# Optimization experiments

Hardware: AMD Instinct MI355X
Metric: run time of the kernel (lower is better)

## Reference

```python
import jax, jax.numpy as jnp
import numpy as np

B, T, X_DIM, H, Y_DIM = 64, 2048, 256, 512, 1

def _lstm_dir(x, lens, w_ih, w_hh, b_ih, b_hh, reverse):
    # x: [B, T, In]; lens: [B] int; w_ih: [4H, In]; w_hh: [4H, H]
    Bb, Tt, _ = x.shape
    Hh = w_hh.shape[-1]
    t_idx = jnp.arange(Tt)
    if reverse:
        # reverse each sequence within its valid length (pack semantics)
        ridx = jnp.clip(lens[:, None] - 1 - t_idx[None, :], 0, Tt - 1)  # [B, T]
        x = jnp.take_along_axis(x, ridx[:, :, None], axis=1)
    valid = (t_idx[None, :] < lens[:, None]).T            # [T, B]
    xT = jnp.swapaxes(x, 0, 1)                            # [T, B, In]
    # hoist the input projection out of the scan (one big GEMM)
    x_proj = jnp.einsum('tbi,gi->tbg', xT, w_ih) + b_ih + b_hh  # [T, B, 4H]
    h0 = jnp.zeros((Bb, Hh), x.dtype)
    c0 = jnp.zeros((Bb, Hh), x.dtype)

    def step(carry, inp):
        h, c = carry
        xp, m = inp                                       # [B,4H], [B]
        g = xp + h @ w_hh.T
        i, f, gg, o = jnp.split(g, 4, axis=-1)            # torch gate order i,f,g,o
        i = jax.nn.sigmoid(i); f = jax.nn.sigmoid(f)
        gg = jnp.tanh(gg); o = jax.nn.sigmoid(o)
        c_new = f * c + i * gg
        h_new = o * jnp.tanh(c_new)
        m = m[:, None]
        h = jnp.where(m, h_new, h)                        # freeze state past seq end
        c = jnp.where(m, c_new, c)
        return (h, c), h

    (h_last, _), outs = jax.lax.scan(step, (h0, c0), (x_proj, valid))
    outs = jnp.swapaxes(outs, 0, 1)                       # [B, T, H]
    if reverse:
        ridx = jnp.clip(lens[:, None] - 1 - t_idx[None, :], 0, Tt - 1)
        outs = jnp.take_along_axis(outs, ridx[:, :, None], axis=1)
    return outs, h_last


def setup_inputs() -> dict:
    key = jax.random.key(0)
    ks = jax.random.split(key, 12)
    s = 1.0 / np.sqrt(H)
    u = lambda k, shp: jax.random.uniform(k, shp, jnp.float32, -s, s)
    seqs = jax.random.normal(ks[0], (B, T, X_DIM), jnp.float32)
    lens = jax.random.randint(ks[1], (B,), 1, T + 1)
    seqs_len = jnp.sort(lens)[::-1].astype(jnp.int64)     # descending, as pack_padded requires
    return {
        'seqs': seqs, 'seqs_len': seqs_len,
        'w_ih_l0': u(ks[2], (2, 4 * H, X_DIM)),   # [dir, 4H, in]
        'w_hh_l0': u(ks[3], (2, 4 * H, H)),
        'b_ih_l0': u(ks[4], (2, 4 * H)),
        'b_hh_l0': u(ks[5], (2, 4 * H)),
        'w_ih_l1': u(ks[6], (2, 4 * H, 2 * H)),
        'w_hh_l1': u(ks[7], (2, 4 * H, H)),
        'b_ih_l1': u(ks[8], (2, 4 * H)),
        'b_hh_l1': u(ks[9], (2, 4 * H)),
        'w_out': u(ks[10], (Y_DIM, 2 * H)),
        'b_out': u(ks[11], (Y_DIM,)),
    }


def reference(seqs, seqs_len, w_ih_l0, w_hh_l0, b_ih_l0, b_hh_l0,
              w_ih_l1, w_hh_l1, b_ih_l1, b_hh_l1, w_out, b_out):
    lens = seqs_len.astype(jnp.int32)
    x = seqs
    h_f = h_b = None
    for (wi, wh, bi, bh) in ((w_ih_l0, w_hh_l0, b_ih_l0, b_hh_l0),
                             (w_ih_l1, w_hh_l1, b_ih_l1, b_hh_l1)):
        out_f, h_f = _lstm_dir(x, lens, wi[0], wh[0], bi[0], bh[0], reverse=False)
        out_b, h_b = _lstm_dir(x, lens, wi[1], wh[1], bi[1], bh[1], reverse=True)
        x = jnp.concatenate([out_f, out_b], axis=-1)      # [B, T, 2H]
    out = jnp.concatenate([h_f, h_b], axis=1)             # last-layer final hidden, [B, 2H]
    out = jax.nn.sigmoid(out @ w_out.T + b_out)           # [B, y_dim]
    return out.squeeze(-1)                                # [B]
```

## Files before the change

### kernel.cpp

```cpp
#include <hip/hip_runtime.h>
#include <stdint.h>
#include <stddef.h>

#define B_  64
#define T_  2048
#define XD  256
#define H_  512
#define G4  2048
#define BT_ (B_*T_)

typedef __attribute__((ext_vector_type(8))) _Float16 f16x8;
typedef __attribute__((ext_vector_type(4))) float f32x4;
typedef __attribute__((ext_vector_type(4))) unsigned int u32x4;
typedef __attribute__((ext_vector_type(4))) unsigned short us4;
typedef __attribute__((ext_vector_type(2))) _Float16 f16x2;

__device__ __attribute__((aligned(256))) unsigned short g_xh[(size_t)BT_*XD];
__device__ __attribute__((aligned(256))) unsigned short g_w1h[(size_t)2*G4*XD];
__device__ __attribute__((aligned(256))) unsigned short g_w2h[(size_t)2*G4*1024];
__device__ __attribute__((aligned(256))) _Float16       g_xproj[(size_t)2*BT_*G4];
__device__ __attribute__((aligned(256))) unsigned short g_out1[(size_t)BT_*1024];
__device__ __attribute__((aligned(256))) unsigned short g_hbuf[2][2][2][B_*H_];
__device__ __attribute__((aligned(256))) float          g_hlast[2][B_*H_];
__device__ __attribute__((aligned(256))) unsigned int   g_flag[2][2][64][32];

__device__ inline unsigned short f2h(float f) {
  _Float16 h = (_Float16)f;
  return __builtin_bit_cast(unsigned short, h);
}
__device__ inline float sigf(float x)  { return 1.f/(1.f + __expf(-x)); }
__device__ inline float tanh_(float x) { return 1.f - 2.f/(__expf(2.f*x) + 1.f); }

__global__ void k_init() {
  unsigned int i = blockIdx.x*256u + threadIdx.x;
  unsigned int stride = gridDim.x*256u;
  unsigned int* hb = (unsigned int*)&g_hbuf[0][0][0][0];
  for (unsigned int j = i; j < sizeof(g_hbuf)/4; j += stride) hb[j] = 0u;
  unsigned int* fl = (unsigned int*)&g_flag[0][0][0][0];
  for (unsigned int j = i; j < sizeof(g_flag)/4; j += stride) fl[j] = 0u;
}

__global__ void k_cvt_x(const float* __restrict__ src) {
  const size_t n4 = (size_t)BT_*XD/4;
  for (size_t j = (size_t)blockIdx.x*blockDim.x + threadIdx.x; j < n4;
       j += (size_t)gridDim.x*blockDim.x) {
    float4 v = ((const float4*)src)[j];
    us4 o = { f2h(v.x), f2h(v.y), f2h(v.z), f2h(v.w) };
    ((us4*)g_xh)[j] = o;
  }
}
__global__ void k_cvt_w1(const float* __restrict__ src) {
  const size_t n4 = (size_t)2*G4*XD/4;
  for (size_t j = (size_t)blockIdx.x*blockDim.x + threadIdx.x; j < n4;
       j += (size_t)gridDim.x*blockDim.x) {
    float4 v = ((const float4*)src)[j];
    us4 o = { f2h(v.x), f2h(v.y), f2h(v.z), f2h(v.w) };
    ((us4*)g_w1h)[j] = o;
  }
}
__global__ void k_cvt_w2(const float* __restrict__ src) {
  const size_t n4 = (size_t)2*G4*1024/4;
  for (size_t j = (size_t)blockIdx.x*blockDim.x + threadIdx.x; j < n4;
       j += (size_t)gridDim.x*blockDim.x) {
    float4 v = ((const float4*)src)[j];
    us4 o = { f2h(v.x), f2h(v.y), f2h(v.z), f2h(v.w) };
    ((us4*)g_w2h)[j] = o;
  }
}

template<int LAYER>
__global__ __launch_bounds__(256) void k_xproj(const float* __restrict__ b_ih,
                                               const float* __restrict__ b_hh,
                                               const int* __restrict__ lens) {
  constexpr int K = (LAYER == 0) ? XD : 1024;
  const unsigned short* __restrict__ Abf = (LAYER == 0) ? g_xh : g_out1;
  const unsigned short* __restrict__ Wbf = (LAYER == 0) ? g_w1h : g_w2h;

  const int m0 = blockIdx.x*128;
  const int n0 = blockIdx.y*128;
  const int d  = blockIdx.z;
  const int bseq = m0 / T_;
  const int t0   = m0 % T_;
  if (t0 >= lens[bseq]) return;

  __shared__ unsigned short As[128*64];
  __shared__ unsigned short Bs[128*64];

  const int tid  = threadIdx.x;
  const int lane = tid & 63;
  const int wv   = tid >> 6;
  const int moff = (wv >> 1)*64;
  const int noff = (wv & 1)*64;

  f32x4 acc[4][4] = {};

  const unsigned short* Ag = Abf + (size_t)m0*K;
  const unsigned short* Wg = Wbf + ((size_t)d*G4 + n0)*K;

  for (int k0 = 0; k0 < K; k0 += 64) {
    __syncthreads();
    #pragma unroll
    for (int p = 0; p < 4; ++p) {
      int sidx = p*256 + tid;
      int row = sidx >> 3;
      int ch  = sidx & 7;
      u32x4 va = *(const u32x4*)(Ag + (size_t)row*K + k0 + ch*8);
      u32x4 vb = *(const u32x4*)(Wg + (size_t)row*K + k0 + ch*8);
      int wb = row*128 + ((ch ^ (row & 7)) << 4);
      *(u32x4*)((char*)As + wb) = va;
      *(u32x4*)((char*)Bs + wb) = vb;
    }
    __syncthreads();
    #pragma unroll
    for (int kt = 0; kt < 2; ++kt) {
      int slot = kt*4 + (lane >> 4);
      f16x8 af[4], bfv[4];
      #pragma unroll
      for (int mt = 0; mt < 4; ++mt) {
        int r = moff + mt*16 + (lane & 15);
        af[mt] = *(const f16x8*)((const char*)As + r*128 + ((slot ^ (r & 7)) << 4));
      }
      #pragma unroll
      for (int nt = 0; nt < 4; ++nt) {
        int r = noff + nt*16 + (lane & 15);
        bfv[nt] = *(const f16x8*)((const char*)Bs + r*128 + ((slot ^ (r & 7)) << 4));
      }
      #pragma unroll
      for (int mt = 0; mt < 4; ++mt)
        #pragma unroll
        for (int nt = 0; nt < 4; ++nt)
          acc[mt][nt] = __builtin_amdgcn_mfma_f32_16x16x32_f16(af[mt], bfv[nt], acc[mt][nt], 0, 0, 0);
    }
  }

  #pragma unroll
  for (int nt = 0; nt < 4; ++nt) {
    const int col = n0 + noff + nt*16 + (lane & 15);
    const float bias = b_ih[d*G4 + col] + b_hh[d*G4 + col];
    #pragma unroll
    for (int mt = 0; mt < 4; ++mt) {
      const int row = m0 + moff + mt*16 + (lane >> 4)*4;
      _Float16* op = g_xproj + ((size_t)d*BT_ + row)*G4 + col;
      #pragma unroll
      for (int j = 0; j < 4; ++j)
        op[(size_t)j*G4] = (_Float16)(acc[mt][nt][j] + bias);
    }
  }
}

template<int LAYER>
__global__ __launch_bounds__(256, 1) void k_scan(const float* __restrict__ w_hh,
                                                 const int* __restrict__ lens) {
  const int dir  = blockIdx.x & 1;
  const int wg   = blockIdx.x >> 1;
  const int tid  = threadIdx.x;
  const int lane = tid & 63;
  const int wv   = tid >> 6;

  __shared__ unsigned short Wl[32*512];
  __shared__ float gs[64*33];

  for (int i = tid; i < 32*256; i += 256) {
    int e = i*2;
    int row = e >> 9;
    int k   = e & 511;
    int gate = row >> 3, hc = row & 7;
    int grow = gate*H_ + wg*8 + hc;
    const float* wsrc = w_hh + ((size_t)dir*G4 + grow)*H_ + k;
    unsigned int pk = (unsigned int)f2h(wsrc[0]) | ((unsigned int)f2h(wsrc[1]) << 16);
    int byte = row*1024 + ((((k*2) >> 4) ^ (row & 7)) << 4) + ((k*2) & 15);
    *(unsigned int*)((char*)Wl + byte) = pk;
  }
  __syncthreads();

  f16x8 b0r[16], b1r[16];
  {
    const int r0 = lane & 15, r1 = 16 + (lane & 15);
    #pragma unroll
    for (int kt = 0; kt < 16; ++kt) {
      int slot = kt*4 + (lane >> 4);
      b0r[kt] = *(const f16x8*)((const char*)Wl + r0*1024 + ((slot ^ (r0 & 7)) << 4));
      b1r[kt] = *(const f16x8*)((const char*)Wl + r1*1024 + ((slot ^ (r1 & 7)) << 4));
    }
  }

  const int myseq = tid >> 2;
  const int hcA   = (tid & 3)*2;
  const int mylen = lens[myseq];
  const int maxlen = lens[0];
  const int col0  = wg*8;
  const int arow  = wv*16 + (lane & 15);
  float c0 = 0.f, c1 = 0.f, h0k = 0.f, h1k = 0.f;
  unsigned int hold = 0u;

  unsigned short* hbuf0 = &g_hbuf[LAYER][dir][0][0];
  unsigned short* hbuf1 = &g_hbuf[LAYER][dir][1][0];
  unsigned int*   flags = &g_flag[LAYER][dir][0][0];

  const unsigned int h_voff  = (unsigned int)(arow*1024 + ((lane >> 4)*16));
  const unsigned int st_voff = (unsigned int)((myseq*H_ + col0 + hcA)*2);
  const unsigned int fl_voff = (unsigned int)(lane*128);

  const char* xbase = (const char*)((const unsigned int*)
      (g_xproj + (((size_t)dir*B_ + myseq)*T_)*G4 + col0) + (hcA >> 1));

  unsigned int r0w, r1w, r2w, r3w;
  {
    int p0 = dir ? (mylen - 1) : 0;
    const char* xr = xbase + (size_t)p0*4096;
    asm volatile("global_load_dword %0, %1, off"             : "=v"(r0w) : "v"(xr) : "memory");
    asm volatile("global_load_dword %0, %1, off offset:1024" : "=v"(r1w) : "v"(xr) : "memory");
    asm volatile("global_load_dword %0, %1, off offset:2048" : "=v"(r2w) : "v"(xr) : "memory");
    asm volatile("global_load_dword %0, %1, off offset:3072" : "=v"(r3w) : "v"(xr) : "memory");
    asm volatile("s_waitcnt vmcnt(0)" ::: "memory");
    __builtin_amdgcn_sched_barrier(0);
  }

  for (int s = 0; s < maxlen; ++s) {
    const unsigned short* hread = (s & 1) ? hbuf1 : hbuf0;
    unsigned short* hwrite      = (s & 1) ? hbuf0 : hbuf1;
    const bool act = s < mylen;

    f16x8 aa[16];
#define HLD(I, OFS) asm volatile("global_load_dwordx4 %0, %1, %2 offset:" OFS " sc1" \
                                 : "=v"(aa[I]) : "v"(h_voff), "s"(hread) : "memory")
    HLD(0,"0");   HLD(1,"64");  HLD(2,"128"); HLD(3,"192");
    HLD(4,"256"); HLD(5,"320"); HLD(6,"384"); HLD(7,"448");
    HLD(8,"512"); HLD(9,"576"); HLD(10,"640"); HLD(11,"704");
    HLD(12,"768"); HLD(13,"832"); HLD(14,"896"); HLD(15,"960");
#undef HLD

    unsigned int n0w, n1w, n2w, n3w;
    {
      int s1 = s + 1;
      int p1 = dir ? (mylen - 1 - s1) : s1;
      p1 = p1 < 0 ? 0 : (p1 > mylen - 1 ? mylen - 1 : p1);
      const char* xr = xbase + (size_t)p1*4096;
      asm volatile("global_load_dword %0, %1, off"             : "=v"(n0w) : "v"(xr) : "memory");
      asm volatile("global_load_dword %0, %1, off offset:1024" : "=v"(n1w) : "v"(xr) : "memory");
      asm volatile("global_load_dword %0, %1, off offset:2048" : "=v"(n2w) : "v"(xr) : "memory");
      asm volatile("global_load_dword %0, %1, off offset:3072" : "=v"(n3w) : "v"(xr) : "memory");
    }
    asm volatile("s_waitcnt vmcnt(4)" ::: "memory");
    __builtin_amdgcn_sched_barrier(0);

    f32x4 a0e = {0.f,0.f,0.f,0.f}, a0o = {0.f,0.f,0.f,0.f};
    f32x4 a1e = {0.f,0.f,0.f,0.f}, a1o = {0.f,0.f,0.f,0.f};
    #pragma unroll
    for (int kt = 0; kt < 16; kt += 2) {
      a0e = __builtin_amdgcn_mfma_f32_16x16x32_f16(aa[kt],   b0r[kt],   a0e, 0, 0, 0);
      a1e = __builtin_amdgcn_mfma_f32_16x16x32_f16(aa[kt],   b1r[kt],   a1e, 0, 0, 0);
      a0o = __builtin_amdgcn_mfma_f32_16x16x32_f16(aa[kt+1], b0r[kt+1], a0o, 0, 0, 0);
      a1o = __builtin_amdgcn_mfma_f32_16x16x32_f16(aa[kt+1], b1r[kt+1], a1o, 0, 0, 0);
    }
    f32x4 acc0 = a0e + a0o;
    f32x4 acc1 = a1e + a1o;

    #pragma unroll
    for (int j = 0; j < 4; ++j) {
      int srow = wv*16 + (lane >> 4)*4 + j;
      gs[srow*33 + (lane & 15)]      = acc0[j];
      gs[srow*33 + 16 + (lane & 15)] = acc1[j];
    }

    {
      f16x2 p0 = __builtin_bit_cast(f16x2, r0w);
      f16x2 p1 = __builtin_bit_cast(f16x2, r1w);
      f16x2 p2 = __builtin_bit_cast(f16x2, r2w);
      f16x2 p3 = __builtin_bit_cast(f16x2, r3w);
      const int q = myseq*33;
      float vi0 = gs[q + hcA]         + (float)p0[0];
      float vi1 = gs[q + hcA + 1]     + (float)p0[1];
      float vf0 = gs[q + 8 + hcA]     + (float)p1[0];
      float vf1 = gs[q + 8 + hcA + 1] + (float)p1[1];
      float vg0 = gs[q + 16 + hcA]    + (float)p2[0];
      float vg1 = gs[q + 16 + hcA+1]  + (float)p2[1];
      float vo0 = gs[q + 24 + hcA]    + (float)p3[0];
      float vo1 = gs[q + 24 + hcA+1]  + (float)p3[1];
      if (act) {
        float i0 = sigf(vi0), f0 = sigf(vf0), G0 = tanh_(vg0), o0 = sigf(vo0);
        float i1 = sigf(vi1), f1 = sigf(vf1), G1 = tanh_(vg1), o1 = sigf(vo1);
        c0 = f0*c0 + i0*G0;
        c1 = f1*c1 + i1*G1;
        h0k = o0*tanh_(c0);
        h1k = o1*tanh_(c1);
        hold = (unsigned int)f2h(h0k) | ((unsigned int)f2h(h1k) << 16);
      }
    }
    r0w = n0w; r1w = n1w; r2w = n2w; r3w = n3w;

    {
      int pos = dir ? (mylen - 1 - s) : s;
      pos = pos < 0 ? 0 : (pos > mylen - 1 ? mylen - 1 : pos);
      if (LAYER == 0) {
        *(unsigned int*)(g_out1 + ((size_t)myseq*T_ + pos)*1024 + dir*H_ + col0 + hcA) = hold;
      } else {
        g_hlast[dir][myseq*H_ + col0 + hcA]     = h0k;
        g_hlast[dir][myseq*H_ + col0 + hcA + 1] = h1k;
      }
    }
    asm volatile("global_store_dword %0, %1, %2 sc1"
                 :: "v"(st_voff), "v"(hold), "s"(hwrite) : "memory");

    asm volatile("s_waitcnt vmcnt(0)\n\ts_barrier" ::: "memory");

    if (tid == 0) {
      unsigned int fv = (unsigned int)(s + 1);
      unsigned int fo = (unsigned int)(wg*128);
      asm volatile("global_store_dword %0, %1, %2 sc1"
                   :: "v"(fo), "v"(fv), "s"(flags) : "memory");
    }
    if (wv == 0) {
      const unsigned int tgt = (unsigned int)(s + 1);
      while (true) {
        unsigned int v;
        asm volatile("global_load_dword %0, %1, %2 sc1"
                     : "=v"(v) : "v"(fl_voff), "s"(flags) : "memory");
        asm volatile("s_waitcnt vmcnt(0)" ::: "memory");
        if (__all(v >= tgt)) break;
        __builtin_amdgcn_s_sleep(1);
      }
    }
    asm volatile("s_barrier" ::: "memory");
  }
}

__global__ void k_final(const float* __restrict__ w_out, const float* __restrict__ b_out,
                        float* __restrict__ out) {
  const int b = blockIdx.x;
  const int tid = threadIdx.x;
  float sum = 0.f;
  for (int k = tid; k < 1024; k += 256) {
    float h = (k < 512) ? g_hlast[0][b*H_ + k] : g_hlast[1][b*H_ + k - 512];
    sum += h * w_out[k];
  }
  __shared__ float red[256];
  red[tid] = sum;
  __syncthreads();
  for (int st = 128; st > 0; st >>= 1) {
    if (tid < st) red[tid] += red[tid + st];
    __syncthreads();
  }
  if (tid == 0) out[b] = 1.f/(1.f + __expf(-(red[0] + b_out[0])));
}

extern "C" void kernel_launch(void* const* d_in, const int* in_sizes, int n_in,
                              void* d_out, int out_size, void* d_ws, size_t ws_size,
                              hipStream_t stream) {
  (void)in_sizes; (void)n_in; (void)d_ws; (void)ws_size; (void)out_size;
  const float* seqs    = (const float*)d_in[0];
  const int*   lens    = (const int*)d_in[1];
  const float* w_ih_l0 = (const float*)d_in[2];
  const float* w_hh_l0 = (const float*)d_in[3];
  const float* b_ih_l0 = (const float*)d_in[4];
  const float* b_hh_l0 = (const float*)d_in[5];
  const float* w_ih_l1 = (const float*)d_in[6];
  const float* w_hh_l1 = (const float*)d_in[7];
  const float* b_ih_l1 = (const float*)d_in[8];
  const float* b_hh_l1 = (const float*)d_in[9];
  const float* w_out   = (const float*)d_in[10];
  const float* b_out   = (const float*)d_in[11];
  float* outp = (float*)d_out;

  hipLaunchKernelGGL(k_init,   dim3(256),  dim3(256), 0, stream);
  hipLaunchKernelGGL(k_cvt_x,  dim3(2048), dim3(256), 0, stream, seqs);
  hipLaunchKernelGGL(k_cvt_w1, dim3(256),  dim3(256), 0, stream, w_ih_l0);
  hipLaunchKernelGGL(k_cvt_w2, dim3(512),  dim3(256), 0, stream, w_ih_l1);

  hipLaunchKernelGGL((k_xproj<0>), dim3(BT_/128, 16, 2), dim3(256), 0, stream,
                     b_ih_l0, b_hh_l0, lens);
  {
    void* args[] = { (void*)&w_hh_l0, (void*)&lens };
    hipError_t e = hipLaunchCooperativeKernel(k_scan<0>, dim3(128), dim3(256), args, 0u, stream);
    (void)e;
  }
  hipLaunchKernelGGL((k_xproj<1>), dim3(BT_/128, 16, 2), dim3(256), 0, stream,
                     b_ih_l1, b_hh_l1, lens);
  {
    void* args[] = { (void*)&w_hh_l1, (void*)&lens };
    hipError_t e = hipLaunchCooperativeKernel(k_scan<1>, dim3(128), dim3(256), args, 0u, stream);
    (void)e;
  }
  hipLaunchKernelGGL(k_final, dim3(64), dim3(256), 0, stream, w_out, b_out, outp);
}
```

Measured before the change: 19.16 ms.

## Reload recurrent weights from LDS each step and prefetch next x-proj after store

Drops the persistent register copies of the recurrent weight fragments (32 f16x8 values) and re-reads them from swizzled LDS on every timestep, cutting register pressure. The prefetch of the next step's input-projection values moves to after the h store, so those loads can overlap the barrier and flag spin. The barrier now waits with vmcnt(4), leaving the prefetch outstanding. The cost is extra LDS traffic on the serial critical path of every step, and the loop-top wait becomes vmcnt(0), which also waits on the prefetch.

```diff
diff --git a/kernel.cpp b/kernel.cpp
--- a/kernel.cpp
+++ b/kernel.cpp
@@ -173,23 +173,13 @@
   }
   __syncthreads();
 
-  f16x8 b0r[16], b1r[16];
-  {
-    const int r0 = lane & 15, r1 = 16 + (lane & 15);
-    #pragma unroll
-    for (int kt = 0; kt < 16; ++kt) {
-      int slot = kt*4 + (lane >> 4);
-      b0r[kt] = *(const f16x8*)((const char*)Wl + r0*1024 + ((slot ^ (r0 & 7)) << 4));
-      b1r[kt] = *(const f16x8*)((const char*)Wl + r1*1024 + ((slot ^ (r1 & 7)) << 4));
-    }
-  }
-
   const int myseq = tid >> 2;
   const int hcA   = (tid & 3)*2;
   const int mylen = lens[myseq];
   const int maxlen = lens[0];
   const int col0  = wg*8;
   const int arow  = wv*16 + (lane & 15);
+  const int r0f   = lane & 15, r1f = 16 + (lane & 15);
   float c0 = 0.f, c1 = 0.f, h0k = 0.f, h1k = 0.f;
   unsigned int hold = 0u;
 
@@ -204,16 +194,14 @@
   const char* xbase = (const char*)((const unsigned int*)
       (g_xproj + (((size_t)dir*B_ + myseq)*T_)*G4 + col0) + (hcA >> 1));
 
-  unsigned int r0w, r1w, r2w, r3w;
+  unsigned int nx0, nx1, nx2, nx3;
   {
     int p0 = dir ? (mylen - 1) : 0;
     const char* xr = xbase + (size_t)p0*4096;
-    asm volatile("global_load_dword %0, %1, off"             : "=v"(r0w) : "v"(xr) : "memory");
-    asm volatile("global_load_dword %0, %1, off offset:1024" : "=v"(r1w) : "v"(xr) : "memory");
-    asm volatile("global_load_dword %0, %1, off offset:2048" : "=v"(r2w) : "v"(xr) : "memory");
-    asm volatile("global_load_dword %0, %1, off offset:3072" : "=v"(r3w) : "v"(xr) : "memory");
-    asm volatile("s_waitcnt vmcnt(0)" ::: "memory");
-    __builtin_amdgcn_sched_barrier(0);
+    asm volatile("global_load_dword %0, %1, off"             : "=v"(nx0) : "v"(xr) : "memory");
+    asm volatile("global_load_dword %0, %1, off offset:1024" : "=v"(nx1) : "v"(xr) : "memory");
+    asm volatile("global_load_dword %0, %1, off offset:2048" : "=v"(nx2) : "v"(xr) : "memory");
+    asm volatile("global_load_dword %0, %1, off offset:3072" : "=v"(nx3) : "v"(xr) : "memory");
   }
 
   for (int s = 0; s < maxlen; ++s) {
@@ -230,19 +218,17 @@
     HLD(12,"768"); HLD(13,"832"); HLD(14,"896"); HLD(15,"960");
 #undef HLD
 
-    unsigned int n0w, n1w, n2w, n3w;
-    {
-      int s1 = s + 1;
-      int p1 = dir ? (mylen - 1 - s1) : s1;
-      p1 = p1 < 0 ? 0 : (p1 > mylen - 1 ? mylen - 1 : p1);
-      const char* xr = xbase + (size_t)p1*4096;
-      asm volatile("global_load_dword %0, %1, off"             : "=v"(n0w) : "v"(xr) : "memory");
-      asm volatile("global_load_dword %0, %1, off offset:1024" : "=v"(n1w) : "v"(xr) : "memory");
-      asm volatile("global_load_dword %0, %1, off offset:2048" : "=v"(n2w) : "v"(xr) : "memory");
-      asm volatile("global_load_dword %0, %1, off offset:3072" : "=v"(n3w) : "v"(xr) : "memory");
-    }
-    asm volatile("s_waitcnt vmcnt(4)" ::: "memory");
+    f16x8 b0r[16], b1r[16];
+    #pragma unroll
+    for (int kt = 0; kt < 16; ++kt) {
+      int slot = kt*4 + (lane >> 4);
+      b0r[kt] = *(const f16x8*)((const char*)Wl + r0f*1024 + ((slot ^ (r0f & 7)) << 4));
+      b1r[kt] = *(const f16x8*)((const char*)Wl + r1f*1024 + ((slot ^ (r1f & 7)) << 4));
+    }
+
+    asm volatile("s_waitcnt vmcnt(0)" ::: "memory");
     __builtin_amdgcn_sched_barrier(0);
+    unsigned int x0 = nx0, x1 = nx1, x2 = nx2, x3 = nx3;
 
     f32x4 a0e = {0.f,0.f,0.f,0.f}, a0o = {0.f,0.f,0.f,0.f};
     f32x4 a1e = {0.f,0.f,0.f,0.f}, a1o = {0.f,0.f,0.f,0.f};
@@ -264,10 +250,10 @@
     }
 
     {
-      f16x2 p0 = __builtin_bit_cast(f16x2, r0w);
-      f16x2 p1 = __builtin_bit_cast(f16x2, r1w);
-      f16x2 p2 = __builtin_bit_cast(f16x2, r2w);
-      f16x2 p3 = __builtin_bit_cast(f16x2, r3w);
+      f16x2 p0 = __builtin_bit_cast(f16x2, x0);
+      f16x2 p1 = __builtin_bit_cast(f16x2, x1);
+      f16x2 p2 = __builtin_bit_cast(f16x2, x2);
+      f16x2 p3 = __builtin_bit_cast(f16x2, x3);
       const int q = myseq*33;
       float vi0 = gs[q + hcA]         + (float)p0[0];
       float vi1 = gs[q + hcA + 1]     + (float)p0[1];
@@ -287,7 +273,6 @@
         hold = (unsigned int)f2h(h0k) | ((unsigned int)f2h(h1k) << 16);
       }
     }
-    r0w = n0w; r1w = n1w; r2w = n2w; r3w = n3w;
 
     {
       int pos = dir ? (mylen - 1 - s) : s;
@@ -302,7 +287,18 @@
     asm volatile("global_store_dword %0, %1, %2 sc1"
                  :: "v"(st_voff), "v"(hold), "s"(hwrite) : "memory");
 
-    asm volatile("s_waitcnt vmcnt(0)\n\ts_barrier" ::: "memory");
+    {
+      int s1 = s + 1;
+      int p1 = dir ? (mylen - 1 - s1) : s1;
+      p1 = p1 < 0 ? 0 : (p1 > mylen - 1 ? mylen - 1 : p1);
+      const char* xr = xbase + (size_t)p1*4096;
+      asm volatile("global_load_dword %0, %1, off"             : "=v"(nx0) : "v"(xr) : "memory");
+      asm volatile("global_load_dword %0, %1, off offset:1024" : "=v"(nx1) : "v"(xr) : "memory");
+      asm volatile("global_load_dword %0, %1, off offset:2048" : "=v"(nx2) : "v"(xr) : "memory");
+      asm volatile("global_load_dword %0, %1, off offset:3072" : "=v"(nx3) : "v"(xr) : "memory");
+    }
+
+    asm volatile("s_waitcnt vmcnt(4)\n\ts_barrier" ::: "memory");
 
     if (tid == 0) {
       unsigned int fv = (unsigned int)(s + 1);
```

Result: no change. 18.90 ms (-1.4%).
